# Kernel optimization log

Measured on AMD Instinct MI355X. Metric: run time of the kernel, lower is better.

Reference implementation:

```python
import jax, jax.numpy as jnp
import numpy as np

EPS = 1e-12  # torch F.normalize eps


def setup_inputs() -> dict:
    key = jax.random.key(0)
    k1, k2, k3 = jax.random.split(key, 3)
    B, way, shot, D, H, W = 64, 5, 1, 640, 5, 5
    nq = 75
    base = jax.random.normal(k1, (B, way, shot, D, H, W), dtype=jnp.float32)
    query = jax.random.normal(k2, (B, nq, D, H, W), dtype=jnp.float32)
    r = jax.random.normal(k3, (2,), dtype=jnp.float32) * 0.1
    return {"base": base, "query": query, "r": r, "neighbor_k": 5}


def reference(base, query, r, neighbor_k):
    B, way, shot, D, H, W = base.shape
    nq = query.shape[1]
    hw = H * W

    # ---- global-cosine branch: spatial-mean descriptors ----
    base_mean = base.reshape(B, way * shot, D, hw).mean(axis=-1)   # [B, way*shot, D]
    query_mean = query.reshape(B, nq, D, hw).mean(axis=-1)         # [B, nq, D]
    bm = base_mean / jnp.maximum(jnp.linalg.norm(base_mean, axis=-1, keepdims=True), EPS)
    qm = query_mean / jnp.maximum(jnp.linalg.norm(query_mean, axis=-1, keepdims=True), EPS)
    logits = jnp.einsum('bqd,bkd->bqk', qm, bm)                    # [B, nq, way*shot]

    # ---- DN4 image-to-class branch (vectorized over the original triple loop) ----
    # query local descriptors: [B, nq, hw, D], L2-normalized over channels
    q = query.reshape(B, nq, D, hw).transpose(0, 1, 3, 2)
    q = q / jnp.linalg.norm(q, axis=-1, keepdims=True)
    # support local descriptors: base_mix [B, way, shot*D, hw], column-normalized
    s = base.reshape(B, way, shot * D, hw)
    s = s / jnp.linalg.norm(s, axis=2, keepdims=True)
    # cosine sims between every query patch and every support patch of each class
    # (requires shot*D == D, i.e. shot == 1, as in the original code)
    sim = jnp.einsum('bqpd,bkdl->bqkpl', q, s)                     # [B, nq, way, hw, hw]
    topk_vals, _ = jax.lax.top_k(sim, neighbor_k)                  # [B, nq, way, hw, k]
    logits_dn4 = topk_vals.sum(axis=(-1, -2)) / neighbor_k         # [B, nq, way]

    return r[0] * logits + r[1] * logits_dn4
```

## Files before the change

kernel.cpp:

```cpp
#include <hip/hip_runtime.h>
#include <hip/hip_bf16.h>
#include <math.h>

#define NB    64
#define WAY   5
#define DCH   640
#define HW    25
#define NQ    75
#define NBK   5
#define EPSN  1e-12f

#define KC    160
#define NCH   (DCH / KC)
#define DG    (KC / 8)
#define ROWS  129
#define QPB   4
#define BPB   ((NQ + QPB - 1) / QPB)

typedef __attribute__((ext_vector_type(8)))  short bf16x8;
typedef __attribute__((ext_vector_type(16))) float f32x16;

__device__ inline ushort f2bf(float f) {
    uint u = __float_as_uint(f);
    return (ushort)((u + 0x7FFFu + ((u >> 16) & 1u)) >> 16);
}

__global__ __launch_bounds__(256) void k_prep(const float* __restrict__ base,
                                              float* __restrict__ invs,
                                              float* __restrict__ invsm)
{
    const int bk = blockIdx.x;
    const float* src = base + (size_t)bk * (DCH * HW);
    __shared__ float lds[DCH * HW];
    __shared__ float red[256];
    const int tid = threadIdx.x;

    const float4* s4 = (const float4*)src;
    float4* l4 = (float4*)lds;
    for (int i = tid; i < (DCH * HW) / 4; i += 256) l4[i] = s4[i];
    __syncthreads();

    if (tid < HW) {
        float ss = 0.f;
        for (int d = 0; d < DCH; ++d) { float v = lds[d * HW + tid]; ss = fmaf(v, v, ss); }
        invs[bk * HW + tid] = rsqrtf(ss);
    }

    float ssq = 0.f;
    for (int d = tid; d < DCH; d += 256) {
        float s = 0.f;
        #pragma unroll
        for (int pp = 0; pp < HW; ++pp) s += lds[d * HW + pp];
        float m = s * (1.0f / HW);
        ssq = fmaf(m, m, ssq);
    }
    red[tid] = ssq;
    __syncthreads();
    for (int s = 128; s > 0; s >>= 1) {
        if (tid < s) red[tid] += red[tid + s];
        __syncthreads();
    }
    if (tid == 0) invsm[bk] = 1.0f / fmaxf(sqrtf(red[0]), EPSN);
}

__global__ __launch_bounds__(256, 2) void k_fused(const float* __restrict__ base,
                                                  const float* __restrict__ query,
                                                  const float* __restrict__ invs,
                                                  const float* __restrict__ invsm,
                                                  const float* __restrict__ r,
                                                  float* __restrict__ out)
{
    __shared__ __align__(16) ushort s_lds[DG * ROWS * 8];
    __shared__ float invs_l[WAY * HW];
    __shared__ float invsm_l[WAY];

    const int tid  = threadIdx.x;
    const int wid  = tid >> 6;
    const int lane = tid & 63;
    const int p    = lane & 31;
    const int hi   = lane >> 5;

    const int wk = (blockIdx.x & 7) * (int)(gridDim.x >> 3) + (blockIdx.x >> 3);
    const int b  = wk / BPB;
    const int qb = wk - b * BPB;
    const int q  = qb * QPB + wid;
    const bool qok = q < NQ;

    if (tid < WAY * HW) invs_l[tid] = invs[b * WAY * HW + tid];
    if (tid < WAY)      invsm_l[tid] = invsm[b * WAY + tid];

    f32x16 acc0 = {}, acc1 = {}, acc2 = {}, acc3 = {}, accg = {};

    const int pc = (p < HW) ? p : (HW - 1);
    const float* qp = query + (size_t)(b * NQ + (qok ? q : 0)) * (DCH * HW) + pc;

    for (int c = 0; c < NCH; ++c) {
        __syncthreads();
        for (int rr = tid; rr < WAY * KC; rr += 256) {
            const int k = rr / KC, dloc = rr - k * KC;
            const float* src = base + ((size_t)(b * WAY + k) * DCH + c * KC + dloc) * HW;
            ushort* dst = &s_lds[(((dloc >> 3) * ROWS) + k * HW) * 8 + (dloc & 7)];
            #pragma unroll
            for (int l = 0; l < HW; ++l) dst[l * 8] = f2bf(src[l]);
        }
        for (int i = tid; i < DG * 3; i += 256) {
            const int dg = i / 3, rz = 125 + (i - dg * 3);
            *(ulonglong2*)&s_lds[(dg * ROWS + rz) * 8] = ulonglong2{0ull, 0ull};
        }
        __syncthreads();

        if (qok) {
            #pragma unroll
            for (int st = 0; st < KC / 16; ++st) {
                const int dg = st * 2 + hi;
                const float* qs = qp + (size_t)(c * KC + st * 16 + hi * 8) * HW;
                bf16x8 bq;
                #pragma unroll
                for (int e = 0; e < 8; ++e) bq[e] = (short)f2bf(qs[e * HW]);
                const bf16x8* arow = (const bf16x8*)&s_lds[(dg * ROWS) * 8];
                bf16x8 a0 = arow[p];
                bf16x8 a1 = arow[32 + p];
                bf16x8 a2 = arow[64 + p];
                bf16x8 a3 = arow[96 + p];
                acc0 = __builtin_amdgcn_mfma_f32_32x32x16_bf16(a0, bq, acc0, 0, 0, 0);
                acc1 = __builtin_amdgcn_mfma_f32_32x32x16_bf16(a1, bq, acc1, 0, 0, 0);
                acc2 = __builtin_amdgcn_mfma_f32_32x32x16_bf16(a2, bq, acc2, 0, 0, 0);
                acc3 = __builtin_amdgcn_mfma_f32_32x32x16_bf16(a3, bq, acc3, 0, 0, 0);
                accg = __builtin_amdgcn_mfma_f32_32x32x16_bf16(bq, bq, accg, 0, 0, 0);
            }
        }
    }
    if (!qok) return;

    const bool pok = p < HW;

    float diag = 0.f;
    #pragma unroll
    for (int rr = 0; rr < 16; ++rr) {
        const int rowb = (rr & 3) + 8 * (rr >> 2);
        diag = ((rowb + 4 * hi) == p) ? accg[rr] : diag;
    }
    diag += __shfl_xor(diag, 32);
    const float invq = rsqrtf(diag);

    float gs[WAY] = {0.f, 0.f, 0.f, 0.f, 0.f};
    float qq = 0.f;
    #pragma unroll
    for (int rr = 0; rr < 16; ++rr) {
        const int rowb = (rr & 3) + 8 * (rr >> 2);
        const float v0 = hi ? 0.f : accg[rr];
        const float v1 = hi ? accg[rr] : 0.f;
        if (rowb < HW)     qq += v0;
        if (rowb + 4 < HW) qq += v1;
    }
#define TILE_SUM(ACC, T)                                            \
    _Pragma("unroll")                                               \
    for (int rr = 0; rr < 16; ++rr) {                               \
        const int s0 = (T) * 32 + (rr & 3) + 8 * (rr >> 2);         \
        const float v0 = hi ? 0.f : ACC[rr];                        \
        const float v1 = hi ? ACC[rr] : 0.f;                        \
        if (s0 < 125)     gs[s0 / 25]       += v0;                  \
        if (s0 + 4 < 125) gs[(s0 + 4) / 25] += v1;                  \
    }
    TILE_SUM(acc0, 0) TILE_SUM(acc1, 1) TILE_SUM(acc2, 2) TILE_SUM(acc3, 3)
#undef TILE_SUM

    if (!pok) {
        qq = 0.f;
        #pragma unroll
        for (int g = 0; g < WAY; ++g) gs[g] = 0.f;
    }
    #pragma unroll
    for (int o = 1; o < 64; o <<= 1) {
        qq += __shfl_xor(qq, o);
        #pragma unroll
        for (int g = 0; g < WAY; ++g) gs[g] += __shfl_xor(gs[g], o);
    }

    float A[64];
    #pragma unroll
    for (int rr = 0; rr < 16; ++rr) {
        A[rr] = acc0[rr]; A[16 + rr] = acc1[rr]; A[32 + rr] = acc2[rr]; A[48 + rr] = acc3[rr];
    }

    float tots[WAY];
    #pragma unroll
    for (int g = 0; g < WAY; ++g) {
        float v[HW];
        #pragma unroll
        for (int j = 0; j < HW; ++j) {
            const int scol = g * HW + j;
            const int t = scol >> 5, row = scol & 31;
            const int hreq = (row >> 2) & 1;
            const int rr = (row & 3) | ((row >> 3) << 2);
            float mine = (hi == hreq) ? A[t * 16 + rr] : 0.f;
            mine += __shfl_xor(mine, 32);
            v[j] = mine * invq * invs_l[scol];
        }
        float gtot = 0.f;
        #pragma unroll
        for (int it = 0; it < NBK; ++it) {
            float m = v[0];
            #pragma unroll
            for (int j = 1; j < HW; ++j) m = fmaxf(m, v[j]);
            gtot += m;
            bool rem = false;
            #pragma unroll
            for (int j = 0; j < HW; ++j) {
                const bool hit = (!rem) && (v[j] == m);
                v[j] = hit ? -3.402823466e38f : v[j];
                rem = rem || hit;
            }
        }
        tots[g] = pok ? gtot : 0.f;
    }
    #pragma unroll
    for (int o = 1; o < 64; o <<= 1) {
        #pragma unroll
        for (int g = 0; g < WAY; ++g) tots[g] += __shfl_xor(tots[g], o);
    }

    const float r0 = r[0], r1 = r[1];
    const float invqm = 1.0f / fmaxf(sqrtf(qq) * (1.0f / HW), EPSN);
    float res[WAY];
    #pragma unroll
    for (int g = 0; g < WAY; ++g)
        res[g] = r0 * gs[g] * (1.0f / 625.0f) * invqm * invsm_l[g]
               + r1 * tots[g] * 0.5f * (1.0f / NBK);

    float ov = res[0];
    ov = (lane == 1) ? res[1] : ov;
    ov = (lane == 2) ? res[2] : ov;
    ov = (lane == 3) ? res[3] : ov;
    ov = (lane == 4) ? res[4] : ov;
    if (lane < WAY) out[(size_t)(b * NQ + q) * WAY + lane] = ov;
}

extern "C" void kernel_launch(void* const* d_in, const int* in_sizes, int n_in,
                              void* d_out, int out_size, void* d_ws, size_t ws_size,
                              hipStream_t stream)
{
    const float* base  = (const float*)d_in[0];
    const float* query = (const float*)d_in[1];
    const float* r     = (const float*)d_in[2];
    float* out = (float*)d_out;

    float* invs  = (float*)d_ws;
    float* invsm = invs + NB * WAY * HW;

    k_prep<<<NB * WAY, 256, 0, stream>>>(base, invs, invsm);
    k_fused<<<NB * BPB, 256, 0, stream>>>(base, query, invs, invsm, r, out);
}
```

Measured before the change: 131.9 us.

## Pretranspose support to bf16 global buffer in prep; stream from global in fused kernel

The prep kernel now also writes the support descriptors as a bf16, d-group-major, column-padded buffer in workspace. The fused kernel drops its per-chunk LDS staging and barriers and reads MFMA A operands straight from that global buffer, which should be L2-resident. Before, each of the 19 blocks per batch converted the same fp32 support data. The query norm now comes from an fp32 sum of squares instead of the Gram diagonal, and loads use nontemporal hints with occupancy raised to 3 blocks per CU. The cost is extra global traffic and one more workspace write.

```diff
diff --git a/kernel.cpp b/kernel.cpp
--- a/kernel.cpp
+++ b/kernel.cpp
@@ -10,15 +10,15 @@
 #define NBK   5
 #define EPSN  1e-12f
 
-#define KC    160
-#define NCH   (DCH / KC)
-#define DG    (KC / 8)
-#define ROWS  129
 #define QPB   4
 #define BPB   ((NQ + QPB - 1) / QPB)
-
-typedef __attribute__((ext_vector_type(8)))  short bf16x8;
-typedef __attribute__((ext_vector_type(16))) float f32x16;
+#define NDG   (DCH / 8)
+#define SCOLS 128
+
+typedef __attribute__((ext_vector_type(8)))  short  bf16x8;
+typedef __attribute__((ext_vector_type(8)))  ushort u16x8;
+typedef __attribute__((ext_vector_type(16))) float  f32x16;
+typedef __attribute__((ext_vector_type(4)))  float  f32x4;
 
 __device__ inline ushort f2bf(float f) {
     uint u = __float_as_uint(f);
@@ -27,17 +27,21 @@
 
 __global__ __launch_bounds__(256) void k_prep(const float* __restrict__ base,
                                               float* __restrict__ invs,
-                                              float* __restrict__ invsm)
+                                              float* __restrict__ invsm,
+                                              ushort* __restrict__ sT)
 {
     const int bk = blockIdx.x;
+    const int b  = bk / WAY;
+    const int k  = bk - b * WAY;
     const float* src = base + (size_t)bk * (DCH * HW);
     __shared__ float lds[DCH * HW];
     __shared__ float red[256];
     const int tid = threadIdx.x;
 
-    const float4* s4 = (const float4*)src;
-    float4* l4 = (float4*)lds;
-    for (int i = tid; i < (DCH * HW) / 4; i += 256) l4[i] = s4[i];
+    const f32x4* s4 = (const f32x4*)src;
+    f32x4* l4 = (f32x4*)lds;
+    for (int i = tid; i < (DCH * HW) / 4; i += 256)
+        l4[i] = __builtin_nontemporal_load(s4 + i);
     __syncthreads();
 
     if (tid < HW) {
@@ -61,16 +65,31 @@
         __syncthreads();
     }
     if (tid == 0) invsm[bk] = 1.0f / fmaxf(sqrtf(red[0]), EPSN);
-}
-
-__global__ __launch_bounds__(256, 2) void k_fused(const float* __restrict__ base,
-                                                  const float* __restrict__ query,
+
+    ushort* dstb = sT + (size_t)b * (NDG * SCOLS * 8);
+    for (int t = tid; t < NDG * HW; t += 256) {
+        const int dg = t / HW, l = t - dg * HW;
+        u16x8 v;
+        #pragma unroll
+        for (int e = 0; e < 8; ++e) v[e] = f2bf(lds[(dg * 8 + e) * HW + l]);
+        *(u16x8*)&dstb[((size_t)dg * SCOLS + k * HW + l) * 8] = v;
+    }
+    if (k == 0) {
+        const u16x8 z = (u16x8)(ushort)0;
+        for (int t = tid; t < NDG * 3; t += 256) {
+            const int dg = t / 3, sc = 125 + (t - dg * 3);
+            *(u16x8*)&dstb[((size_t)dg * SCOLS + sc) * 8] = z;
+        }
+    }
+}
+
+__global__ __launch_bounds__(256, 3) void k_fused(const float* __restrict__ query,
+                                                  const ushort* __restrict__ sT,
                                                   const float* __restrict__ invs,
                                                   const float* __restrict__ invsm,
                                                   const float* __restrict__ r,
                                                   float* __restrict__ out)
 {
-    __shared__ __align__(16) ushort s_lds[DG * ROWS * 8];
     __shared__ float invs_l[WAY * HW];
     __shared__ float invsm_l[WAY];
 
@@ -88,60 +107,43 @@
 
     if (tid < WAY * HW) invs_l[tid] = invs[b * WAY * HW + tid];
     if (tid < WAY)      invsm_l[tid] = invsm[b * WAY + tid];
+    __syncthreads();
+    if (!qok) return;
 
     f32x16 acc0 = {}, acc1 = {}, acc2 = {}, acc3 = {}, accg = {};
+    float ssq = 0.f;
 
     const int pc = (p < HW) ? p : (HW - 1);
-    const float* qp = query + (size_t)(b * NQ + (qok ? q : 0)) * (DCH * HW) + pc;
-
-    for (int c = 0; c < NCH; ++c) {
-        __syncthreads();
-        for (int rr = tid; rr < WAY * KC; rr += 256) {
-            const int k = rr / KC, dloc = rr - k * KC;
-            const float* src = base + ((size_t)(b * WAY + k) * DCH + c * KC + dloc) * HW;
-            ushort* dst = &s_lds[(((dloc >> 3) * ROWS) + k * HW) * 8 + (dloc & 7)];
-            #pragma unroll
-            for (int l = 0; l < HW; ++l) dst[l * 8] = f2bf(src[l]);
-        }
-        for (int i = tid; i < DG * 3; i += 256) {
-            const int dg = i / 3, rz = 125 + (i - dg * 3);
-            *(ulonglong2*)&s_lds[(dg * ROWS + rz) * 8] = ulonglong2{0ull, 0ull};
-        }
-        __syncthreads();
-
-        if (qok) {
-            #pragma unroll
-            for (int st = 0; st < KC / 16; ++st) {
-                const int dg = st * 2 + hi;
-                const float* qs = qp + (size_t)(c * KC + st * 16 + hi * 8) * HW;
-                bf16x8 bq;
-                #pragma unroll
-                for (int e = 0; e < 8; ++e) bq[e] = (short)f2bf(qs[e * HW]);
-                const bf16x8* arow = (const bf16x8*)&s_lds[(dg * ROWS) * 8];
-                bf16x8 a0 = arow[p];
-                bf16x8 a1 = arow[32 + p];
-                bf16x8 a2 = arow[64 + p];
-                bf16x8 a3 = arow[96 + p];
-                acc0 = __builtin_amdgcn_mfma_f32_32x32x16_bf16(a0, bq, acc0, 0, 0, 0);
-                acc1 = __builtin_amdgcn_mfma_f32_32x32x16_bf16(a1, bq, acc1, 0, 0, 0);
-                acc2 = __builtin_amdgcn_mfma_f32_32x32x16_bf16(a2, bq, acc2, 0, 0, 0);
-                acc3 = __builtin_amdgcn_mfma_f32_32x32x16_bf16(a3, bq, acc3, 0, 0, 0);
-                accg = __builtin_amdgcn_mfma_f32_32x32x16_bf16(bq, bq, accg, 0, 0, 0);
-            }
-        }
-    }
-    if (!qok) return;
+    const float* qp = query + (size_t)(b * NQ + q) * (DCH * HW) + pc;
+    const ushort* sTb = sT + (size_t)b * (NDG * SCOLS * 8);
+
+    #pragma unroll 4
+    for (int st = 0; st < DCH / 16; ++st) {
+        const int dg = st * 2 + hi;
+        const float* qs = qp + (size_t)(st * 16 + hi * 8) * HW;
+        bf16x8 bq;
+        #pragma unroll
+        for (int e = 0; e < 8; ++e) {
+            const float v = __builtin_nontemporal_load(qs + e * HW);
+            ssq = fmaf(v, v, ssq);
+            bq[e] = (short)f2bf(v);
+        }
+        const bf16x8* arow = (const bf16x8*)(sTb + (size_t)dg * SCOLS * 8);
+        const bf16x8 a0 = arow[p];
+        const bf16x8 a1 = arow[32 + p];
+        const bf16x8 a2 = arow[64 + p];
+        const bf16x8 a3 = arow[96 + p];
+        acc0 = __builtin_amdgcn_mfma_f32_32x32x16_bf16(a0, bq, acc0, 0, 0, 0);
+        acc1 = __builtin_amdgcn_mfma_f32_32x32x16_bf16(a1, bq, acc1, 0, 0, 0);
+        acc2 = __builtin_amdgcn_mfma_f32_32x32x16_bf16(a2, bq, acc2, 0, 0, 0);
+        acc3 = __builtin_amdgcn_mfma_f32_32x32x16_bf16(a3, bq, acc3, 0, 0, 0);
+        accg = __builtin_amdgcn_mfma_f32_32x32x16_bf16(bq, bq, accg, 0, 0, 0);
+    }
 
     const bool pok = p < HW;
 
-    float diag = 0.f;
-    #pragma unroll
-    for (int rr = 0; rr < 16; ++rr) {
-        const int rowb = (rr & 3) + 8 * (rr >> 2);
-        diag = ((rowb + 4 * hi) == p) ? accg[rr] : diag;
-    }
-    diag += __shfl_xor(diag, 32);
-    const float invq = rsqrtf(diag);
+    ssq += __shfl_xor(ssq, 32);
+    const float invq = rsqrtf(ssq);
 
     float gs[WAY] = {0.f, 0.f, 0.f, 0.f, 0.f};
     float qq = 0.f;
@@ -245,9 +247,10 @@
     const float* r     = (const float*)d_in[2];
     float* out = (float*)d_out;
 
-    float* invs  = (float*)d_ws;
-    float* invsm = invs + NB * WAY * HW;
-
-    k_prep<<<NB * WAY, 256, 0, stream>>>(base, invs, invsm);
-    k_fused<<<NB * BPB, 256, 0, stream>>>(base, query, invs, invsm, r, out);
-}
+    float* invs   = (float*)d_ws;
+    float* invsm  = invs + NB * WAY * HW;
+    ushort* sT    = (ushort*)((float*)d_ws + 16384);
+
+    k_prep<<<NB * WAY, 256, 0, stream>>>(base, invs, invsm, sT);
+    k_fused<<<NB * BPB, 256, 0, stream>>>(query, sT, invs, invsm, r, out);
+}
```

New measurement: 134.2 us. No clear change (+1.7%).
